# Kernel optimization log

Measured on AMD Instinct MI355X. Metric: run time of the kernel, lower is better.

## Reference

```python
import jax, jax.numpy as jnp
import numpy as np

NUM_NODES = 19
RESOLUTION = 256
K_KNN = 3
EDGE_TOP_PERC = 0.5
RESIDUAL_W = 0.1
HIDDEN = 128
INPUT_DIM = 32


def _w(k, shape, fan):
    return jax.random.normal(k, shape, jnp.float32) / np.sqrt(fan)


def setup_inputs() -> dict:
    key = jax.random.key(0)
    ks = jax.random.split(key, 12)
    D, H = INPUT_DIM, HIDDEN
    return {
        "x": jax.random.normal(ks[0], (16 * NUM_NODES, 2048, D), jnp.float32),
        # GRU layer 0 (pytorch gate order r,z,n)
        "Wih0": _w(ks[1], (3 * H, D), D), "Whh0": _w(ks[2], (3 * H, H), H),
        "bih0": jnp.zeros(3 * H, jnp.float32), "bhh0": jnp.zeros(3 * H, jnp.float32),
        # GRU layer 1
        "Wih1": _w(ks[3], (3 * H, H), H), "Whh1": _w(ks[4], (3 * H, H), H),
        "bih1": jnp.zeros(3 * H, jnp.float32), "bhh1": jnp.zeros(3 * H, jnp.float32),
        # self-attention graph learner
        "Wq": _w(ks[5], (H, H), H), "Wk": _w(ks[6], (H, H), H),
        # SAGEConv: lin_l (neighbors, with bias) + lin_r (root)
        "Wl": _w(ks[7], (H, H), H), "Wr": _w(ks[8], (H, H), H),
        "b_sage": jnp.zeros(H, jnp.float32),
        # classifier
        "Wc": _w(ks[9], (1, H), H), "bc": jnp.zeros(1, jnp.float32),
    }


def gru_layer(x, Wih, Whh, bih, bhh):
    """x: (B,T,D) -> (B,T,H), pytorch nn.GRU gate order (r,z,n)."""
    H = Whh.shape[1]

    def step(h, xt):
        gi = xt @ Wih.T + bih          # (B,3H)
        gh = h @ Whh.T + bhh
        i_r, i_z, i_n = jnp.split(gi, 3, axis=-1)
        h_r, h_z, h_n = jnp.split(gh, 3, axis=-1)
        r = jax.nn.sigmoid(i_r + h_r)
        z = jax.nn.sigmoid(i_z + h_z)
        n = jnp.tanh(i_n + r * h_n)
        h_new = (1.0 - z) * n + z * h
        return h_new, h_new

    h0 = jnp.zeros((x.shape[0], H), x.dtype)
    _, ys = jax.lax.scan(step, h0, jnp.swapaxes(x, 0, 1))
    return jnp.swapaxes(ys, 0, 1)


def graphs4mer_forward(x, Wih0, Whh0, bih0, bhh0, Wih1, Whh1, bih1, bhh1,
                       Wq, Wk, Wl, Wr, b_sage, Wc, bc):
    B_total, T, _ = x.shape
    batch = B_total // NUM_NODES
    # temporal model: 2-layer GRU
    h = gru_layer(x, Wih0, Whh0, bih0, bhh0)
    h = gru_layer(h, Wih1, Whh1, bih1, bhh1)
    H = h.shape[-1]
    num_dyn = T // RESOLUTION
    # (batch, N, T, H) -> mean over each resolution window -> (batch, num_dyn, N, H)
    h = h.reshape(batch, NUM_NODES, num_dyn, RESOLUTION, H).mean(axis=3)
    xg = jnp.transpose(h, (0, 2, 1, 3)).reshape(batch * num_dyn, NUM_NODES, H)

    Bp, N = xg.shape[0], NUM_NODES
    I = jnp.eye(N, dtype=xg.dtype)

    # --- KNN cosine graph ---
    xn = xg / jnp.linalg.norm(xg, axis=-1, keepdims=True)
    sim = jnp.einsum('bnd,bmd->bnm', xn, xn)
    knn_val, knn_ind = jax.lax.top_k(sim, K_KNN)
    bi = jnp.arange(Bp)[:, None, None]
    ri = jnp.arange(N)[None, :, None]
    adj_knn = jnp.zeros_like(sim).at[bi, ri, knn_ind].set(knn_val)
    adj_knn = jnp.maximum(adj_knn, 0.0)
    adj_knn = (adj_knn + adj_knn.swapaxes(1, 2)) * 0.5   # undirected
    adj_knn = adj_knn * (1.0 - I) + I                    # force diag = 1

    # --- self-attention graph learner ---
    q = xg @ Wq.T
    k = xg @ Wk.T
    attn = jax.nn.softmax(jnp.einsum('bnd,bmd->bnm', q, k) / np.sqrt(H).astype(np.float32), axis=-1)
    attn = (attn + attn.swapaxes(1, 2)) * 0.5

    adj = RESIDUAL_W * adj_knn + (1.0 - RESIDUAL_W) * attn

    # --- prune: keep top edge_top_perc of entries per graph ---
    Kcut = int(N * N * EDGE_TOP_PERC)
    sorted_desc = -jnp.sort(-adj.reshape(Bp, -1), axis=-1)
    thr = sorted_desc[:, Kcut][:, None, None]
    adj = jnp.where(adj > thr, adj, 0.0)

    # --- feature smoothing regularization: tr(X^T L X)/F^2 ---
    d = adj.sum(-1)
    dis = jnp.where(d > 0, d ** -0.5, 0.0)
    L = I - dis[:, :, None] * adj * dis[:, None, :]
    mat = jnp.einsum('bnf,bnm,bmg->bfg', xg, L, xg) / float(H ** 2)
    reg = jnp.einsum('bff->b', mat).mean()

    # --- GraphSAGE conv on pruned graph (self loops removed, mean aggregation) ---
    adj_ns = adj * (1.0 - I)
    mask = (adj_ns > 0).astype(xg.dtype)
    deg = jnp.maximum(mask.sum(-1, keepdims=True), 1.0)
    agg = jnp.einsum('bnm,bmd->bnd', mask, xg) / deg
    out = jax.nn.relu(agg @ Wl.T + b_sage + xg @ Wr.T)

    # temporal mean pool over dynamic graphs, sum pool over nodes, classify
    out = out.reshape(batch, num_dyn, N, H).mean(axis=1).sum(axis=1)
    logits = out @ Wc.T + bc
    return logits, reg


def reference(x, Wih0, Whh0, bih0, bhh0, Wih1, Whh1, bih1, bhh1,
              Wq, Wk, Wl, Wr, b_sage, Wc, bc):
    return graphs4mer_forward(x, Wih0, Whh0, bih0, bhh0, Wih1, Whh1, bih1, bhh1,
                              Wq, Wk, Wl, Wr, b_sage, Wc, bc)
```

## Files before the change

### kernel.cpp

```cpp
#include <hip/hip_runtime.h>
#include <hip/hip_bf16.h>


#define NSEQ   304
#define TT     2048
#define HH     128
#define NNODE  19
#define NDYN   8
#define NGRAPH 128
#define NBLK   76
#define PITCH  136

typedef __bf16 bf16x8 __attribute__((ext_vector_type(8)));
typedef float  f32x4  __attribute__((ext_vector_type(4)));

static __device__ __forceinline__ f32x4 mfma16(bf16x8 a, bf16x8 b, f32x4 c) {
  return __builtin_amdgcn_mfma_f32_16x16x32_bf16(a, b, c, 0, 0, 0);
}

static __device__ __forceinline__ float pickq(f32x4 v, bool qb0, bool qb1) {
  const float a = qb0 ? v[1] : v[0];
  const float b = qb0 ? v[3] : v[2];
  return qb1 ? b : a;
}

static __device__ __forceinline__ float gate_step(
    float cr, float cz, float cn, float cm,
    float nBr, float nBz, float bin, float bhn, float hp)
{
  const float er = __builtin_amdgcn_exp2f(__builtin_fmaf(cr, -1.4426950408889634f, nBr));
  const float ez = __builtin_amdgcn_exp2f(__builtin_fmaf(cz, -1.4426950408889634f, nBz));
  const float r  = __builtin_amdgcn_rcpf(1.f + er);
  const float z  = __builtin_amdgcn_rcpf(1.f + ez);
  const float gn = __builtin_fmaf(r, cm + bhn, cn + bin);
  const float en = __builtin_amdgcn_exp2f(gn * 2.8853900817779268f);
  const float nn = __builtin_fmaf(__builtin_amdgcn_rcpf(1.f + en), -2.f, 1.f);
  return __builtin_fmaf(z, hp - nn, nn);
}

__global__ void wprep_kernel(const float* __restrict__ src, __bf16* __restrict__ dst,
                             int K, int nk)
{
  const int i = blockIdx.x * 256 + threadIdx.x;
  const int total = 8 * 3 * nk * 64;
  if (i >= total) return;
  const int l = i & 63;
  int rest = i >> 6;
  const int kc = rest % nk; rest /= nk;
  const int gs = rest % 3;
  const int w  = rest / 3;
  const int row = 128 * gs + 16 * w + (l & 15);
  const float* s = src + (size_t)row * K + kc * 32 + (l >> 4) * 8;
  bf16x8 v;
  #pragma unroll
  for (int u = 0; u < 8; ++u) v[u] = (__bf16)s[u];
  *(bf16x8*)&dst[(size_t)i * 8] = v;
}

__global__ void xprep_kernel(const float* __restrict__ x, __bf16* __restrict__ xb)
{
  const int i = blockIdx.x * 256 + threadIdx.x;
  if (i >= NNODE * TT * 64) return;
  const int l = i & 63;
  const int t = (i >> 6) & (TT - 1);
  const int g = i >> 17;
  const float* s = x + ((size_t)(g * 16 + (l & 15)) * TT + t) * 32 + (l >> 4) * 8;
  bf16x8 v;
  #pragma unroll
  for (int u = 0; u < 8; ++u) v[u] = (__bf16)s[u];
  *(bf16x8*)&xb[(size_t)i * 8] = v;
}

__global__ __launch_bounds__(512) __attribute__((amdgpu_waves_per_eu(2, 2)))
void gru2_kernel(
    const __bf16* __restrict__ xb,
    const __bf16* __restrict__ wI0, const __bf16* __restrict__ wH0,
    const __bf16* __restrict__ wI1, const __bf16* __restrict__ wH1,
    const float* __restrict__ bih0, const float* __restrict__ bhh0,
    const float* __restrict__ bih1, const float* __restrict__ bhh1,
    float* __restrict__ xg)
{
  __shared__ __align__(16) __bf16 sH0[2][16 * PITCH];
  __shared__ __align__(16) __bf16 sH1[2][16 * PITCH];

  const int tid = threadIdx.x;
  const int w   = tid >> 6;
  const int l   = tid & 63;
  const int lm  = l & 15;
  const int lq  = l >> 4;
  const int gb  = blockIdx.x;
  const int gg  = gb >> 2;
  const int q0  = gb & 3;
  const bool qb0 = (q0 & 1) != 0;
  const bool qb1 = (q0 & 2) != 0;
  const int j   = 16 * w + lm;
  const int aoff = lm * PITCH + lq * 8;
  const f32x4 z4 = {0.f, 0.f, 0.f, 0.f};

  bf16x8 bI0[3], bH0[3][4], bI1[3][4], bH1[3][4];
  #pragma unroll
  for (int gs = 0; gs < 3; ++gs)
    bI0[gs] = *(const bf16x8*)&wI0[(size_t)((w * 3 + gs) * 64 + l) * 8];
  #pragma unroll
  for (int gs = 0; gs < 3; ++gs)
    #pragma unroll
    for (int kc = 0; kc < 4; ++kc) {
      const size_t fi = (size_t)(((w * 3 + gs) * 4 + kc) * 64 + l) * 8;
      bH0[gs][kc] = *(const bf16x8*)&wH0[fi];
      bI1[gs][kc] = *(const bf16x8*)&wI1[fi];
      bH1[gs][kc] = *(const bf16x8*)&wH1[fi];
    }

  const float L2E = 1.4426950408889634f;
  const float nBr0 = -L2E * (bih0[j] + bhh0[j]);
  const float nBz0 = -L2E * (bih0[128 + j] + bhh0[128 + j]);
  const float bin0 = bih0[256 + j], bhn0 = bhh0[256 + j];
  const float nBr1 = -L2E * (bih1[j] + bhh1[j]);
  const float nBz1 = -L2E * (bih1[128 + j] + bhh1[128 + j]);
  const float bin1 = bih1[256 + j], bhn1 = bhh1[256 + j];

  for (int i = tid; i < 16 * PITCH; i += 512) {
    sH0[0][i] = (__bf16)0.f; sH0[1][i] = (__bf16)0.f;
    sH1[0][i] = (__bf16)0.f; sH1[1][i] = (__bf16)0.f;
  }

  const int myrow = lq * 4 + q0;
  const int woff  = myrow * PITCH + j;
  const int seq   = gg * 16 + myrow;
  const int bidx  = seq / NNODE;
  const int node  = seq - bidx * NNODE;

  float h0p = 0.f, h1p = 0.f, hsum = 0.f;

  const __bf16* xrow = xb + (size_t)gg * TT * 512 + l * 8;
  bf16x8 a0 = *(const bf16x8*)xrow;
  __syncthreads();

  for (int t = 0; t < TT; ++t) {
    __bf16*       h0w = sH0[t & 1];
    const __bf16* h0r = sH0[(t + 1) & 1];
    __bf16*       h1w = sH1[(t + 1) & 1];
    const __bf16* h1r = sH1[t & 1];

    bf16x8 ah0[4], ah1[4];
    #pragma unroll
    for (int kc = 0; kc < 4; ++kc) ah0[kc] = *(const bf16x8*)&h0r[aoff + kc * 32];
    #pragma unroll
    for (int kc = 0; kc < 4; ++kc) ah1[kc] = *(const bf16x8*)&h1r[aoff + kc * 32];

    bf16x8 a0n = *(const bf16x8*)(xrow + (size_t)((t + 1) & (TT - 1)) * 512);

    f32x4 Dr = z4, Dz = z4, Dn = z4, Dm = z4;
    if (t > 0) {
      #pragma unroll
      for (int kc = 0; kc < 4; ++kc) {
        Dr = mfma16(ah0[kc], bI1[0][kc], Dr);
        Dz = mfma16(ah0[kc], bI1[1][kc], Dz);
        Dn = mfma16(ah0[kc], bI1[2][kc], Dn);
      }
      #pragma unroll
      for (int kc = 0; kc < 4; ++kc) {
        Dr = mfma16(ah1[kc], bH1[0][kc], Dr);
        Dz = mfma16(ah1[kc], bH1[1][kc], Dz);
        Dm = mfma16(ah1[kc], bH1[2][kc], Dm);
      }
    }

    f32x4 Cr = mfma16(a0, bI0[0], z4);
    f32x4 Cz = mfma16(a0, bI0[1], z4);
    f32x4 Cn = mfma16(a0, bI0[2], z4);
    f32x4 Cm = z4;
    #pragma unroll
    for (int kc = 0; kc < 4; ++kc) {
      Cr = mfma16(ah0[kc], bH0[0][kc], Cr);
      Cz = mfma16(ah0[kc], bH0[1][kc], Cz);
      Cm = mfma16(ah0[kc], bH0[2][kc], Cm);
    }

    {
      const float h = gate_step(pickq(Cr, qb0, qb1), pickq(Cz, qb0, qb1),
                                pickq(Cn, qb0, qb1), pickq(Cm, qb0, qb1),
                                nBr0, nBz0, bin0, bhn0, h0p);
      h0p = h;
      h0w[woff] = (__bf16)h;
    }
    if (t > 0) {
      const float h = gate_step(pickq(Dr, qb0, qb1), pickq(Dz, qb0, qb1),
                                pickq(Dn, qb0, qb1), pickq(Dm, qb0, qb1),
                                nBr1, nBz1, bin1, bhn1, h1p);
      h1p = h;
      hsum += h;
      h1w[woff] = (__bf16)h;
      const int s = t - 1;
      if ((s & 255) == 255) {
        const int win = s >> 8;
        xg[((size_t)(bidx * NDYN + win) * NNODE + node) * HH + j] =
            hsum * (1.f / 256.f);
        hsum = 0.f;
      }
    }
    a0 = a0n;
    __syncthreads();
  }

  {
    const __bf16* h0r = sH0[1];
    const __bf16* h1r = sH1[0];
    bf16x8 ah0[4], ah1[4];
    #pragma unroll
    for (int kc = 0; kc < 4; ++kc) ah0[kc] = *(const bf16x8*)&h0r[aoff + kc * 32];
    #pragma unroll
    for (int kc = 0; kc < 4; ++kc) ah1[kc] = *(const bf16x8*)&h1r[aoff + kc * 32];
    f32x4 Dr = z4, Dz = z4, Dn = z4, Dm = z4;
    #pragma unroll
    for (int kc = 0; kc < 4; ++kc) {
      Dr = mfma16(ah0[kc], bI1[0][kc], Dr);
      Dz = mfma16(ah0[kc], bI1[1][kc], Dz);
      Dn = mfma16(ah0[kc], bI1[2][kc], Dn);
    }
    #pragma unroll
    for (int kc = 0; kc < 4; ++kc) {
      Dr = mfma16(ah1[kc], bH1[0][kc], Dr);
      Dz = mfma16(ah1[kc], bH1[1][kc], Dz);
      Dm = mfma16(ah1[kc], bH1[2][kc], Dm);
    }
    const float h = gate_step(pickq(Dr, qb0, qb1), pickq(Dz, qb0, qb1),
                              pickq(Dn, qb0, qb1), pickq(Dm, qb0, qb1),
                              nBr1, nBz1, bin1, bhn1, h1p);
    hsum += h;
    xg[((size_t)(bidx * NDYN + 7) * NNODE + node) * HH + j] =
        hsum * (1.f / 256.f);
  }
}

static __device__ __forceinline__ float blockReduce256(float v, float* sRed)
{
  const int tid = threadIdx.x;
  __syncthreads();
  sRed[tid] = v;
  __syncthreads();
  #pragma unroll
  for (int st = 128; st >= 1; st >>= 1) {
    if (tid < st) sRed[tid] += sRed[tid + st];
    __syncthreads();
  }
  return sRed[0];
}

__global__ __launch_bounds__(256) void graph_kernel(
    const float* __restrict__ xg,
    const float* __restrict__ Wq, const float* __restrict__ Wk,
    const float* __restrict__ Wl, const float* __restrict__ Wr,
    const float* __restrict__ bs, const float* __restrict__ Wc,
    float* __restrict__ out)
{
  const int tid = threadIdx.x;
  const int bp = blockIdx.x;

  __shared__ float sX[NNODE * HH];
  __shared__ float sQ[NNODE * HH];
  __shared__ float sK[NNODE * HH];
  __shared__ float sG[NNODE * NNODE];
  __shared__ float sA[NNODE * NNODE];
  __shared__ float sS[NNODE * NNODE];
  __shared__ float sNorm[NNODE];
  __shared__ float sDis[NNODE];
  __shared__ float sDeg[NNODE];
  __shared__ float sThr;
  __shared__ float sRed[256];

  for (int idx = tid; idx < NNODE * HH; idx += 256)
    sX[idx] = xg[(size_t)bp * NNODE * HH + idx];
  __syncthreads();

  if (tid < NNODE) {
    float acc = 0.f;
    const float* xv = &sX[tid * HH];
    #pragma unroll 4
    for (int d = 0; d < HH; ++d) acc += xv[d] * xv[d];
    sNorm[tid] = 1.f / sqrtf(acc);
  }
  for (int e = tid; e < NNODE * NNODE; e += 256) {
    const int n = e / NNODE, m = e % NNODE;
    float acc = 0.f;
    const float* a = &sX[n * HH];
    const float* b = &sX[m * HH];
    #pragma unroll 4
    for (int d = 0; d < HH; ++d) acc += a[d] * b[d];
    sG[e] = acc;
  }
  for (int e = tid; e < NNODE * NNODE; e += 256) sA[e] = 0.f;
  __syncthreads();

  if (tid < NNODE) {
    const int r = tid;
    const float nr = sNorm[r];
    float v0 = -1e30f, v1 = -1e30f, v2 = -1e30f;
    int i0 = 0, i1 = 0, i2 = 0;
    for (int m = 0; m < NNODE; ++m) {
      const float v = sG[r * NNODE + m] * nr * sNorm[m];
      if (v > v0)      { v2 = v1; i2 = i1; v1 = v0; i1 = i0; v0 = v; i0 = m; }
      else if (v > v1) { v2 = v1; i2 = i1; v1 = v;  i1 = m; }
      else if (v > v2) { v2 = v;  i2 = m; }
    }
    sA[r * NNODE + i0] = fmaxf(v0, 0.f);
    sA[r * NNODE + i1] = fmaxf(v1, 0.f);
    sA[r * NNODE + i2] = fmaxf(v2, 0.f);
  }
  __syncthreads();

  {
    float t0 = 0.f, t1 = 0.f;
    if (tid < 361) {
      const int n = tid / NNODE, m = tid % NNODE;
      t0 = (n == m) ? 1.f : 0.5f * (sA[n * NNODE + m] + sA[m * NNODE + n]);
    }
    if (tid + 256 < 361) {
      const int e = tid + 256;
      const int n = e / NNODE, m = e % NNODE;
      t1 = (n == m) ? 1.f : 0.5f * (sA[n * NNODE + m] + sA[m * NNODE + n]);
    }
    __syncthreads();
    if (tid < 361) sA[tid] = t0;
    if (tid + 256 < 361) sA[tid + 256] = t1;
  }

  for (int o = tid; o < NNODE * HH; o += 256) {
    const int n = o >> 7, hh = o & 127;
    float aq = 0.f, ak = 0.f;
    const float* xv = &sX[n * HH];
    const float* wq = &Wq[hh * HH];
    const float* wk = &Wk[hh * HH];
    #pragma unroll 4
    for (int d = 0; d < HH; ++d) { const float xx = xv[d]; aq += xx * wq[d]; ak += xx * wk[d]; }
    sQ[o] = aq; sK[o] = ak;
  }
  __syncthreads();

  for (int e = tid; e < NNODE * NNODE; e += 256) {
    const int n = e / NNODE, m = e % NNODE;
    float acc = 0.f;
    const float* a = &sQ[n * HH];
    const float* b = &sK[m * HH];
    #pragma unroll 4
    for (int d = 0; d < HH; ++d) acc += a[d] * b[d];
    sS[e] = acc * 0.08838834764831845f;
  }
  __syncthreads();
  if (tid < NNODE) {
    const int r = tid;
    float mx = -1e30f;
    for (int m = 0; m < NNODE; ++m) mx = fmaxf(mx, sS[r * NNODE + m]);
    float sum = 0.f;
    for (int m = 0; m < NNODE; ++m) sum += expf(sS[r * NNODE + m] - mx);
    const float inv = 1.f / sum;
    for (int m = 0; m < NNODE; ++m)
      sS[r * NNODE + m] = expf(sS[r * NNODE + m] - mx) * inv;
  }
  __syncthreads();

  for (int e = tid; e < NNODE * NNODE; e += 256) {
    const int n = e / NNODE, m = e % NNODE;
    sA[e] = 0.1f * sA[e] + 0.45f * (sS[n * NNODE + m] + sS[m * NNODE + n]);
  }
  __syncthreads();

  for (int e = tid; e < NNODE * NNODE; e += 256) {
    const float v = sA[e];
    int cg = 0, ce = 0;
    for (int f = 0; f < NNODE * NNODE; ++f) {
      const float u = sA[f];
      cg += (u > v);
      ce += (u == v);
    }
    if (cg <= 180 && cg + ce > 180) sThr = v;
  }
  __syncthreads();
  {
    const float thr = sThr;
    for (int e = tid; e < NNODE * NNODE; e += 256)
      sA[e] = (sA[e] > thr) ? sA[e] : 0.f;
  }
  __syncthreads();

  if (tid < NNODE) {
    const int r = tid;
    float dsum = 0.f;
    int cnt = 0;
    for (int m = 0; m < NNODE; ++m) {
      const float v = sA[r * NNODE + m];
      dsum += v;
      if (m != r && v > 0.f) ++cnt;
    }
    sDis[r] = (dsum > 0.f) ? 1.f / sqrtf(dsum) : 0.f;
    sDeg[r] = (float)(cnt < 1 ? 1 : cnt);
  }
  __syncthreads();

  float regp = 0.f;
  for (int e = tid; e < NNODE * NNODE; e += 256) {
    const int n = e / NNODE, m = e % NNODE;
    const float Lnm = ((n == m) ? 1.f : 0.f) - sDis[n] * sDis[m] * sA[e];
    regp += Lnm * sG[e];
  }
  {
    const float tr = blockReduce256(regp, sRed);
    if (tid == 0)
      atomicAdd(out + 16, tr * (1.f / (16384.f * (float)NGRAPH)));
  }
  __syncthreads();

  for (int o = tid; o < NNODE * HH; o += 256) {
    const int n = o >> 7, d = o & 127;
    float acc = 0.f;
    for (int m = 0; m < NNODE; ++m)
      if (m != n && sA[n * NNODE + m] > 0.f) acc += sX[m * HH + d];
    sQ[o] = acc / sDeg[n];
  }
  __syncthreads();

  float lgp = 0.f;
  for (int o = tid; o < NNODE * HH; o += 256) {
    const int n = o >> 7, hh = o & 127;
    float acc = bs[hh];
    const float* av = &sQ[n * HH];
    const float* xv = &sX[n * HH];
    const float* wl = &Wl[hh * HH];
    const float* wr = &Wr[hh * HH];
    #pragma unroll 4
    for (int d = 0; d < HH; ++d) acc += av[d] * wl[d] + xv[d] * wr[d];
    lgp += fmaxf(acc, 0.f) * Wc[hh];
  }
  {
    const float tot = blockReduce256(lgp, sRed);
    if (tid == 0)
      atomicAdd(out + (bp >> 3), tot * 0.125f);
  }
}

__global__ void init_out_kernel(float* __restrict__ out, const float* __restrict__ bc)
{
  const int i = threadIdx.x;
  if (i < 16) out[i] = bc[0];
  else if (i == 16) out[16] = 0.f;
}

extern "C" void kernel_launch(void* const* d_in, const int* in_sizes, int n_in,
                              void* d_out, int out_size, void* d_ws, size_t ws_size,
                              hipStream_t stream)
{
  const float* x    = (const float*)d_in[0];
  const float* Wih0 = (const float*)d_in[1];
  const float* Whh0 = (const float*)d_in[2];
  const float* bih0 = (const float*)d_in[3];
  const float* bhh0 = (const float*)d_in[4];
  const float* Wih1 = (const float*)d_in[5];
  const float* Whh1 = (const float*)d_in[6];
  const float* bih1 = (const float*)d_in[7];
  const float* bhh1 = (const float*)d_in[8];
  const float* Wq   = (const float*)d_in[9];
  const float* Wk   = (const float*)d_in[10];
  const float* Wl   = (const float*)d_in[11];
  const float* Wr   = (const float*)d_in[12];
  const float* bsg  = (const float*)d_in[13];
  const float* Wc   = (const float*)d_in[14];
  const float* bc   = (const float*)d_in[15];
  float* out = (float*)d_out;

  const size_t XB  = (size_t)NNODE * TT * 512 * sizeof(__bf16);
  const size_t WI0 = (size_t)8 * 3 * 64 * 8 * sizeof(__bf16);
  const size_t WH  = (size_t)8 * 3 * 4 * 64 * 8 * sizeof(__bf16);
  char* p = (char*)d_ws;
  __bf16* xb  = (__bf16*)p;            p += XB;
  __bf16* wI0 = (__bf16*)p;            p += WI0;
  __bf16* wH0 = (__bf16*)p;            p += WH;
  __bf16* wI1 = (__bf16*)p;            p += WH;
  __bf16* wH1 = (__bf16*)p;            p += WH;
  float*  xg  = (float*)p;

  init_out_kernel<<<1, 64, 0, stream>>>(out, bc);
  wprep_kernel<<<6, 256, 0, stream>>>(Wih0, wI0, 32, 1);
  wprep_kernel<<<24, 256, 0, stream>>>(Whh0, wH0, 128, 4);
  wprep_kernel<<<24, 256, 0, stream>>>(Wih1, wI1, 128, 4);
  wprep_kernel<<<24, 256, 0, stream>>>(Whh1, wH1, 128, 4);
  xprep_kernel<<<(NNODE * TT * 64 + 255) / 256, 256, 0, stream>>>(x, xb);
  gru2_kernel<<<NBLK, 512, 0, stream>>>(
      xb, wI0, wH0, wI1, wH1, bih0, bhh0, bih1, bhh1, xg);
  graph_kernel<<<NGRAPH, 256, 0, stream>>>(xg, Wq, Wk, Wl, Wr, bsg, Wc, out);
}
```

Before: 2.017 ms.

## Swizzle GRU hidden-state LDS layout and template quadrant selection

Replaces the padded LDS hidden-state buffers with an unpadded XOR-swizzled layout, so the MFMA operand reads and the scalar writes avoid bank conflicts without the padding. Makes the per-block quadrant index a template parameter, dispatched through a switch, so the accumulator lane pick becomes a compile-time index instead of runtime selects. It also moves the layer-0 input MFMAs earlier and reorders the two gate computations within the step. The cost is a larger code footprint from four instantiations, and the reordering may change register pressure.

```diff
diff --git a/kernel.cpp b/kernel.cpp
--- a/kernel.cpp
+++ b/kernel.cpp
@@ -9,19 +9,12 @@
 #define NDYN   8
 #define NGRAPH 128
 #define NBLK   76
-#define PITCH  136
 
 typedef __bf16 bf16x8 __attribute__((ext_vector_type(8)));
 typedef float  f32x4  __attribute__((ext_vector_type(4)));
 
 static __device__ __forceinline__ f32x4 mfma16(bf16x8 a, bf16x8 b, f32x4 c) {
   return __builtin_amdgcn_mfma_f32_16x16x32_bf16(a, b, c, 0, 0, 0);
-}
-
-static __device__ __forceinline__ float pickq(f32x4 v, bool qb0, bool qb1) {
-  const float a = qb0 ? v[1] : v[0];
-  const float b = qb0 ? v[3] : v[2];
-  return qb1 ? b : a;
 }
 
 static __device__ __forceinline__ float gate_step(
@@ -71,30 +64,22 @@
   *(bf16x8*)&xb[(size_t)i * 8] = v;
 }
 
-__global__ __launch_bounds__(512) __attribute__((amdgpu_waves_per_eu(2, 2)))
-void gru2_kernel(
+template<int Q0>
+static __device__ __forceinline__ void gru_body(
     const __bf16* __restrict__ xb,
     const __bf16* __restrict__ wI0, const __bf16* __restrict__ wH0,
     const __bf16* __restrict__ wI1, const __bf16* __restrict__ wH1,
     const float* __restrict__ bih0, const float* __restrict__ bhh0,
     const float* __restrict__ bih1, const float* __restrict__ bhh1,
-    float* __restrict__ xg)
-{
-  __shared__ __align__(16) __bf16 sH0[2][16 * PITCH];
-  __shared__ __align__(16) __bf16 sH1[2][16 * PITCH];
-
+    float* __restrict__ xg,
+    __bf16* s0a, __bf16* s0b, __bf16* s1a, __bf16* s1b, int gg)
+{
   const int tid = threadIdx.x;
   const int w   = tid >> 6;
   const int l   = tid & 63;
   const int lm  = l & 15;
   const int lq  = l >> 4;
-  const int gb  = blockIdx.x;
-  const int gg  = gb >> 2;
-  const int q0  = gb & 3;
-  const bool qb0 = (q0 & 1) != 0;
-  const bool qb1 = (q0 & 2) != 0;
   const int j   = 16 * w + lm;
-  const int aoff = lm * PITCH + lq * 8;
   const f32x4 z4 = {0.f, 0.f, 0.f, 0.f};
 
   bf16x8 bI0[3], bH0[3][4], bI1[3][4], bH1[3][4];
@@ -119,13 +104,19 @@
   const float nBz1 = -L2E * (bih1[128 + j] + bhh1[128 + j]);
   const float bin1 = bih1[256 + j], bhn1 = bhh1[256 + j];
 
-  for (int i = tid; i < 16 * PITCH; i += 512) {
-    sH0[0][i] = (__bf16)0.f; sH0[1][i] = (__bf16)0.f;
-    sH1[0][i] = (__bf16)0.f; sH1[1][i] = (__bf16)0.f;
-  }
-
-  const int myrow = lq * 4 + q0;
-  const int woff  = myrow * PITCH + j;
+  for (int i = tid; i < 16 * HH; i += 512) {
+    s0a[i] = (__bf16)0.f; s0b[i] = (__bf16)0.f;
+    s1a[i] = (__bf16)0.f; s1b[i] = (__bf16)0.f;
+  }
+
+  const int sw = lm & 7;
+  int eo[4];
+  #pragma unroll
+  for (int kc = 0; kc < 4; ++kc)
+    eo[kc] = lm * HH + ((((kc << 2) | lq) ^ sw) << 3);
+
+  const int myrow = lq * 4 + Q0;
+  const int woff  = myrow * HH + (((j >> 3) ^ (myrow & 7)) << 3) + (j & 7);
   const int seq   = gg * 16 + myrow;
   const int bidx  = seq / NNODE;
   const int node  = seq - bidx * NNODE;
@@ -137,18 +128,22 @@
   __syncthreads();
 
   for (int t = 0; t < TT; ++t) {
-    __bf16*       h0w = sH0[t & 1];
-    const __bf16* h0r = sH0[(t + 1) & 1];
-    __bf16*       h1w = sH1[(t + 1) & 1];
-    const __bf16* h1r = sH1[t & 1];
+    __bf16*       h0w = (t & 1) ? s0b : s0a;
+    const __bf16* h0r = (t & 1) ? s0a : s0b;
+    __bf16*       h1w = (t & 1) ? s1a : s1b;
+    const __bf16* h1r = (t & 1) ? s1b : s1a;
 
     bf16x8 ah0[4], ah1[4];
     #pragma unroll
-    for (int kc = 0; kc < 4; ++kc) ah0[kc] = *(const bf16x8*)&h0r[aoff + kc * 32];
-    #pragma unroll
-    for (int kc = 0; kc < 4; ++kc) ah1[kc] = *(const bf16x8*)&h1r[aoff + kc * 32];
+    for (int kc = 0; kc < 4; ++kc) ah0[kc] = *(const bf16x8*)&h0r[eo[kc]];
+    #pragma unroll
+    for (int kc = 0; kc < 4; ++kc) ah1[kc] = *(const bf16x8*)&h1r[eo[kc]];
 
     bf16x8 a0n = *(const bf16x8*)(xrow + (size_t)((t + 1) & (TT - 1)) * 512);
+
+    f32x4 Cr = mfma16(a0, bI0[0], z4);
+    f32x4 Cz = mfma16(a0, bI0[1], z4);
+    f32x4 Cn = mfma16(a0, bI0[2], z4);
 
     f32x4 Dr = z4, Dz = z4, Dn = z4, Dm = z4;
     if (t > 0) {
@@ -166,9 +161,6 @@
       }
     }
 
-    f32x4 Cr = mfma16(a0, bI0[0], z4);
-    f32x4 Cz = mfma16(a0, bI0[1], z4);
-    f32x4 Cn = mfma16(a0, bI0[2], z4);
     f32x4 Cm = z4;
     #pragma unroll
     for (int kc = 0; kc < 4; ++kc) {
@@ -177,16 +169,8 @@
       Cm = mfma16(ah0[kc], bH0[2][kc], Cm);
     }
 
-    {
-      const float h = gate_step(pickq(Cr, qb0, qb1), pickq(Cz, qb0, qb1),
-                                pickq(Cn, qb0, qb1), pickq(Cm, qb0, qb1),
-                                nBr0, nBz0, bin0, bhn0, h0p);
-      h0p = h;
-      h0w[woff] = (__bf16)h;
-    }
     if (t > 0) {
-      const float h = gate_step(pickq(Dr, qb0, qb1), pickq(Dz, qb0, qb1),
-                                pickq(Dn, qb0, qb1), pickq(Dm, qb0, qb1),
+      const float h = gate_step(Dr[Q0], Dz[Q0], Dn[Q0], Dm[Q0],
                                 nBr1, nBz1, bin1, bhn1, h1p);
       h1p = h;
       hsum += h;
@@ -199,18 +183,24 @@
         hsum = 0.f;
       }
     }
+    {
+      const float h = gate_step(Cr[Q0], Cz[Q0], Cn[Q0], Cm[Q0],
+                                nBr0, nBz0, bin0, bhn0, h0p);
+      h0p = h;
+      h0w[woff] = (__bf16)h;
+    }
     a0 = a0n;
     __syncthreads();
   }
 
   {
-    const __bf16* h0r = sH0[1];
-    const __bf16* h1r = sH1[0];
+    const __bf16* h0r = s0b;
+    const __bf16* h1r = s1a;
     bf16x8 ah0[4], ah1[4];
     #pragma unroll
-    for (int kc = 0; kc < 4; ++kc) ah0[kc] = *(const bf16x8*)&h0r[aoff + kc * 32];
-    #pragma unroll
-    for (int kc = 0; kc < 4; ++kc) ah1[kc] = *(const bf16x8*)&h1r[aoff + kc * 32];
+    for (int kc = 0; kc < 4; ++kc) ah0[kc] = *(const bf16x8*)&h0r[eo[kc]];
+    #pragma unroll
+    for (int kc = 0; kc < 4; ++kc) ah1[kc] = *(const bf16x8*)&h1r[eo[kc]];
     f32x4 Dr = z4, Dz = z4, Dn = z4, Dm = z4;
     #pragma unroll
     for (int kc = 0; kc < 4; ++kc) {
@@ -224,12 +214,35 @@
       Dz = mfma16(ah1[kc], bH1[1][kc], Dz);
       Dm = mfma16(ah1[kc], bH1[2][kc], Dm);
     }
-    const float h = gate_step(pickq(Dr, qb0, qb1), pickq(Dz, qb0, qb1),
-                              pickq(Dn, qb0, qb1), pickq(Dm, qb0, qb1),
+    const float h = gate_step(Dr[Q0], Dz[Q0], Dn[Q0], Dm[Q0],
                               nBr1, nBz1, bin1, bhn1, h1p);
     hsum += h;
     xg[((size_t)(bidx * NDYN + 7) * NNODE + node) * HH + j] =
         hsum * (1.f / 256.f);
+  }
+}
+
+__global__ __launch_bounds__(512) __attribute__((amdgpu_waves_per_eu(2, 2)))
+void gru2_kernel(
+    const __bf16* __restrict__ xb,
+    const __bf16* __restrict__ wI0, const __bf16* __restrict__ wH0,
+    const __bf16* __restrict__ wI1, const __bf16* __restrict__ wH1,
+    const float* __restrict__ bih0, const float* __restrict__ bhh0,
+    const float* __restrict__ bih1, const float* __restrict__ bhh1,
+    float* __restrict__ xg)
+{
+  __shared__ __align__(16) __bf16 sH0[2][16 * HH];
+  __shared__ __align__(16) __bf16 sH1[2][16 * HH];
+  const int gg = blockIdx.x >> 2;
+  switch (blockIdx.x & 3) {
+    case 0: gru_body<0>(xb, wI0, wH0, wI1, wH1, bih0, bhh0, bih1, bhh1, xg,
+                        sH0[0], sH0[1], sH1[0], sH1[1], gg); break;
+    case 1: gru_body<1>(xb, wI0, wH0, wI1, wH1, bih0, bhh0, bih1, bhh1, xg,
+                        sH0[0], sH0[1], sH1[0], sH1[1], gg); break;
+    case 2: gru_body<2>(xb, wI0, wH0, wI1, wH1, bih0, bhh0, bih1, bhh1, xg,
+                        sH0[0], sH0[1], sH1[0], sH1[1], gg); break;
+    default: gru_body<3>(xb, wI0, wH0, wI1, wH1, bih0, bhh0, bih1, bhh1, xg,
+                         sH0[0], sH0[1], sH1[0], sH1[1], gg); break;
   }
 }
 
@@ -481,8 +494,8 @@
   init_out_kernel<<<1, 64, 0, stream>>>(out, bc);
   wprep_kernel<<<6, 256, 0, stream>>>(Wih0, wI0, 32, 1);
   wprep_kernel<<<24, 256, 0, stream>>>(Whh0, wH0, 128, 4);
+  wprep_kernel<<<24, 256, 0, stream>>>(Whh1, wH1, 128, 4);
   wprep_kernel<<<24, 256, 0, stream>>>(Wih1, wI1, 128, 4);
-  wprep_kernel<<<24, 256, 0, stream>>>(Whh1, wH1, 128, 4);
   xprep_kernel<<<(NNODE * TT * 64 + 255) / 256, 256, 0, stream>>>(x, xb);
   gru2_kernel<<<NBLK, 512, 0, stream>>>(
       xb, wI0, wH0, wI1, wH1, bih0, bhh0, bih1, bhh1, xg);
```

Measured after the change: 2.040 ms. No clear change (+1.1%).
